# Kernel tuning notes

Hardware: AMD Instinct MI355X
Metric: run time of the kernel (lower is better)

## Reference

```python
import jax, jax.numpy as jnp
import numpy as np

STRIDE = 1
PADDING = 1

def setup_inputs() -> dict:
    key = jax.random.key(0)
    k1, k2, k3 = jax.random.split(key, 3)
    N, C_in, H, W = 32, 128, 56, 56
    C_out, K = 256, 3
    inputs = jax.random.normal(k1, (N, C_in, H, W), dtype=jnp.float32)
    # trunc_normal(std=0.1) approximated by clipped normal
    filters = jnp.clip(jax.random.normal(k2, (C_out, C_in, K, K), dtype=jnp.float32) * 0.1, -0.2, 0.2)
    bias = jnp.clip(jax.random.normal(k3, (C_out,), dtype=jnp.float32) * 0.1, -0.2, 0.2)
    return {"inputs": inputs, "filters": filters, "bias": bias}

def reference(inputs, filters, bias):
    # Equivalent of the quadruple-loop conv: standard cross-correlation,
    # NCHW input, OIHW filters, stride/padding from module config.
    out = jax.lax.conv_general_dilated(
        inputs, filters,
        window_strides=(STRIDE, STRIDE),
        padding=[(PADDING, PADDING), (PADDING, PADDING)],
        dimension_numbers=("NCHW", "OIHW", "NCHW"),
    )
    out = out + bias[None, :, None, None]
    return out
```

## Files before the change

### kernel.cpp

```cpp
#include <hip/hip_runtime.h>

#define CIN    128
#define HH     56
#define WW_    56
#define NBATCH 32
#define COUT   256
#define KTOT   1152
#define PLANE  3136
#define HP     58
#define BM     128
#define BN     128
#define BK     64

#define WB_OFF   0
#define XP_OFF   (1u << 20)

typedef __attribute__((ext_vector_type(8))) short bf16x8;
typedef __attribute__((ext_vector_type(4))) float f32x4;

__device__ __forceinline__ unsigned short f2bf(float f) {
    unsigned int u = __builtin_bit_cast(unsigned int, f);
    u += 0x7fffu + ((u >> 16) & 1u);
    return (unsigned short)(u >> 16);
}

__device__ __forceinline__ void gl_lds16(const void* g, void* l) {
    __builtin_amdgcn_global_load_lds(
        (const __attribute__((address_space(1))) void*)g,
        (__attribute__((address_space(3))) void*)l, 16, 0, 0);
}

__global__ void wprep(const float* __restrict__ w, unsigned short* __restrict__ wb) {
    const int o = blockIdx.x;
    const int t = threadIdx.x;
    const float* src = w + (size_t)o * KTOT;
    unsigned short* dst = wb + (size_t)o * KTOT;
    #pragma unroll
    for (int e = 0; e < 5; ++e) {
        const int idx = t + e * 256;
        if (idx < KTOT) {
            const int ci  = idx / 9;
            const int tap = idx - ci * 9;
            dst[tap * 128 + ci] = f2bf(src[idx]);
        }
    }
}

__global__ __launch_bounds__(256)
void xprep(const float* __restrict__ in, unsigned short* __restrict__ xp) {
    const int b  = blockIdx.x;
    const int n  = b / HP;
    const int ho = b - n * HP;
    const int t  = threadIdx.x;
    uint4* orow = (uint4*)(xp + (((size_t)n * HP + ho) * HP) * CIN);

    if (ho == 0 || ho == HP - 1) {
        #pragma unroll
        for (int e = 0; e < 4; ++e) {
            const int idx = t + e * 256;
            if (idx < 928) orow[idx] = (uint4){0u, 0u, 0u, 0u};
        }
        return;
    }

    __shared__ unsigned short L[CIN * 57];
    const int h  = ho - 1;
    const int w  = t & 63;
    const int cb = t >> 6;
    if (w < WW_) {
        const float* ib = in + ((size_t)n * CIN) * PLANE + (size_t)h * WW_ + w;
        #pragma unroll
        for (int e = 0; e < 32; ++e) {
            const int ci = cb * 32 + e;
            L[ci * 57 + w] = f2bf(ib[(size_t)ci * PLANE]);
        }
    }
    __syncthreads();

    #pragma unroll
    for (int e = 0; e < 4; ++e) {
        const int idx = t + e * 256;
        if (idx < 928) {
            const int wo = idx >> 4;
            const int ch = idx & 15;
            uint4 pk = {0u, 0u, 0u, 0u};
            if (wo >= 1 && wo <= WW_) {
                const int wi = wo - 1;
                unsigned v[8];
                #pragma unroll
                for (int i = 0; i < 8; ++i)
                    v[i] = L[(ch * 8 + i) * 57 + wi];
                pk.x = v[0] | (v[1] << 16);
                pk.y = v[2] | (v[3] << 16);
                pk.z = v[4] | (v[5] << 16);
                pk.w = v[6] | (v[7] << 16);
            }
            orow[idx] = pk;
        }
    }
}

__global__ __launch_bounds__(256, 2)
void conv_mfma(const unsigned short* __restrict__ wb,
               const unsigned short* __restrict__ xp,
               const float* __restrict__ bias,
               float* __restrict__ out)
{
    __shared__ __align__(16) unsigned short Asm_[BM * BK];
    __shared__ __align__(16) unsigned short Bsm_[BN * BK];

    const int t    = threadIdx.x;
    const int pix0 = blockIdx.x * BN;
    const int c0   = blockIdx.y * BM;

    const int slot = t & 7;
    const int r32  = t >> 3;
    const int swiz = (slot ^ (r32 & 7)) * 16;

    const char* aBase = (const char*)wb + (size_t)(c0 + r32) * (KTOT * 2) + swiz;
    const char* bBase[4];
    #pragma unroll
    for (int p = 0; p < 4; ++p) {
        const int pix = pix0 + r32 + p * 32;
        const int n   = pix / PLANE;
        const int rem = pix - n * PLANE;
        const int h   = rem / WW_;
        const int w   = rem - h * WW_;
        bBase[p] = (const char*)xp + ((size_t)(n * HP + h) * HP + w) * (CIN * 2) + swiz;
    }

    const int lane = t & 63;
    const int wave = t >> 6;
    const int wm   = (wave & 1) * 64;
    const int wn   = (wave >> 1) * 64;
    const int lr   = lane & 15;
    const int quad = lane >> 4;
    const int rmod = lr & 7;

    f32x4 acc[4][4];
    #pragma unroll
    for (int i = 0; i < 4; ++i)
        #pragma unroll
        for (int j = 0; j < 4; ++j)
            acc[i][j] = (f32x4){0.f, 0.f, 0.f, 0.f};

    char* const asmb = (char*)Asm_;
    char* const bsmb = (char*)Bsm_;

    for (int tap = 0; tap < 9; ++tap) {
        const int toff = ((tap / 3) * HP + (tap % 3)) * (CIN * 2);
        for (int ci0b = 0; ci0b < 256; ci0b += 128) {
            const int abyte = tap * 256 + ci0b;
            #pragma unroll
            for (int p = 0; p < 4; ++p)
                gl_lds16(aBase + (size_t)p * 32 * (KTOT * 2) + abyte, asmb + p * 4096 + t * 16);
            #pragma unroll
            for (int p = 0; p < 4; ++p)
                gl_lds16(bBase[p] + toff + ci0b, bsmb + p * 4096 + t * 16);
            __syncthreads();

            #pragma unroll
            for (int kk = 0; kk < 2; ++kk) {
                bf16x8 af[4], bfr[4];
                #pragma unroll
                for (int i = 0; i < 4; ++i) {
                    const int r = wm + i * 16 + lr;
                    const int phys = ((kk * 4 + quad) ^ rmod) * 16;
                    af[i] = *(const bf16x8*)(asmb + r * 128 + phys);
                }
                #pragma unroll
                for (int j = 0; j < 4; ++j) {
                    const int r = wn + j * 16 + lr;
                    const int phys = ((kk * 4 + quad) ^ rmod) * 16;
                    bfr[j] = *(const bf16x8*)(bsmb + r * 128 + phys);
                }
                #pragma unroll
                for (int i = 0; i < 4; ++i)
                    #pragma unroll
                    for (int j = 0; j < 4; ++j)
                        acc[i][j] = __builtin_amdgcn_mfma_f32_16x16x32_bf16(af[i], bfr[j], acc[i][j], 0, 0, 0);
            }
            __syncthreads();
        }
    }

    #pragma unroll
    for (int j = 0; j < 4; ++j) {
        const int pg    = pix0 + wn + j * 16 + lr;
        const int ni    = pg / PLANE;
        const int inner = pg - ni * PLANE;
        float* op = out + (size_t)ni * (COUT * PLANE) + inner;
        #pragma unroll
        for (int i = 0; i < 4; ++i) {
            const int crow = c0 + wm + i * 16 + quad * 4;
            #pragma unroll
            for (int r = 0; r < 4; ++r)
                op[(size_t)(crow + r) * PLANE] = acc[i][j][r] + bias[crow + r];
        }
    }
}

extern "C" void kernel_launch(void* const* d_in, const int* in_sizes, int n_in,
                              void* d_out, int out_size, void* d_ws, size_t ws_size,
                              hipStream_t stream) {
    const float* in   = (const float*)d_in[0];
    const float* wt   = (const float*)d_in[1];
    const float* bias = (const float*)d_in[2];
    float* out        = (float*)d_out;

    unsigned short* wb = (unsigned short*)((char*)d_ws + WB_OFF);
    unsigned short* xp = (unsigned short*)((char*)d_ws + XP_OFF);

    wprep<<<COUT, 256, 0, stream>>>(wt, wb);
    xprep<<<NBATCH * HP, 256, 0, stream>>>(in, xp);

    dim3 grid((NBATCH * PLANE) / BN, COUT / BM);
    conv_mfma<<<grid, 256, 0, stream>>>(wb, xp, bias, out);
}
```

Measured before the change: 208.9 us.

## Fuse prep kernels, vectorize input loads, raise occupancy, use nontemporal output stores

Result: slower. 259.4 us (+24.2%).

```diff
diff --git a/kernel.cpp b/kernel.cpp
--- a/kernel.cpp
+++ b/kernel.cpp
@@ -14,6 +14,7 @@
 
 #define WB_OFF   0
 #define XP_OFF   (1u << 20)
+#define LSTR     66
 
 typedef __attribute__((ext_vector_type(8))) short bf16x8;
 typedef __attribute__((ext_vector_type(4))) float f32x4;
@@ -30,28 +31,32 @@
         (__attribute__((address_space(3))) void*)l, 16, 0, 0);
 }
 
-__global__ void wprep(const float* __restrict__ w, unsigned short* __restrict__ wb) {
-    const int o = blockIdx.x;
+__global__ __launch_bounds__(256)
+void prep(const float* __restrict__ in, const float* __restrict__ wt,
+          unsigned short* __restrict__ xp, unsigned short* __restrict__ wb) {
+    const int b = blockIdx.x;
     const int t = threadIdx.x;
-    const float* src = w + (size_t)o * KTOT;
-    unsigned short* dst = wb + (size_t)o * KTOT;
-    #pragma unroll
-    for (int e = 0; e < 5; ++e) {
-        const int idx = t + e * 256;
-        if (idx < KTOT) {
-            const int ci  = idx / 9;
-            const int tap = idx - ci * 9;
-            dst[tap * 128 + ci] = f2bf(src[idx]);
-        }
-    }
-}
-
-__global__ __launch_bounds__(256)
-void xprep(const float* __restrict__ in, unsigned short* __restrict__ xp) {
-    const int b  = blockIdx.x;
+
+    if (b >= NBATCH * HP) {
+        const int o0 = (b - NBATCH * HP) * 8;
+        for (int oo = 0; oo < 8; ++oo) {
+            const float* src = wt + (size_t)(o0 + oo) * KTOT;
+            unsigned short* dst = wb + (size_t)(o0 + oo) * KTOT;
+            #pragma unroll
+            for (int e = 0; e < 5; ++e) {
+                const int idx = t + e * 256;
+                if (idx < KTOT) {
+                    const int ci  = idx / 9;
+                    const int tap = idx - ci * 9;
+                    dst[tap * 128 + ci] = f2bf(src[idx]);
+                }
+            }
+        }
+        return;
+    }
+
     const int n  = b / HP;
     const int ho = b - n * HP;
-    const int t  = threadIdx.x;
     uint4* orow = (uint4*)(xp + (((size_t)n * HP + ho) * HP) * CIN);
 
     if (ho == 0 || ho == HP - 1) {
@@ -63,16 +68,20 @@
         return;
     }
 
-    __shared__ unsigned short L[CIN * 57];
+    __shared__ unsigned short L[CIN * LSTR];
     const int h  = ho - 1;
-    const int w  = t & 63;
-    const int cb = t >> 6;
-    if (w < WW_) {
-        const float* ib = in + ((size_t)n * CIN) * PLANE + (size_t)h * WW_ + w;
-        #pragma unroll
-        for (int e = 0; e < 32; ++e) {
-            const int ci = cb * 32 + e;
-            L[ci * 57 + w] = f2bf(ib[(size_t)ci * PLANE]);
+    const int f4 = t & 15;
+    const int cg = t >> 4;
+    if (f4 < 14) {
+        const float* rowb = in + ((size_t)n * CIN) * PLANE + (size_t)h * WW_;
+        #pragma unroll
+        for (int g = 0; g < 8; ++g) {
+            const int ci = cg + g * 16;
+            const float4 v = *(const float4*)(rowb + (size_t)ci * PLANE + f4 * 4);
+            unsigned lo = (unsigned)f2bf(v.x) | ((unsigned)f2bf(v.y) << 16);
+            unsigned hi = (unsigned)f2bf(v.z) | ((unsigned)f2bf(v.w) << 16);
+            *(unsigned*)&L[ci * LSTR + f4 * 4]     = lo;
+            *(unsigned*)&L[ci * LSTR + f4 * 4 + 2] = hi;
         }
     }
     __syncthreads();
@@ -89,7 +98,7 @@
                 unsigned v[8];
                 #pragma unroll
                 for (int i = 0; i < 8; ++i)
-                    v[i] = L[(ch * 8 + i) * 57 + wi];
+                    v[i] = L[(ch * 8 + i) * LSTR + wi];
                 pk.x = v[0] | (v[1] << 16);
                 pk.y = v[2] | (v[3] << 16);
                 pk.z = v[4] | (v[5] << 16);
@@ -100,7 +109,7 @@
     }
 }
 
-__global__ __launch_bounds__(256, 2)
+__global__ __launch_bounds__(256, 4)
 void conv_mfma(const unsigned short* __restrict__ wb,
                const unsigned short* __restrict__ xp,
                const float* __restrict__ bias,
@@ -195,7 +204,8 @@
             const int crow = c0 + wm + i * 16 + quad * 4;
             #pragma unroll
             for (int r = 0; r < 4; ++r)
-                op[(size_t)(crow + r) * PLANE] = acc[i][j][r] + bias[crow + r];
+                __builtin_nontemporal_store(acc[i][j][r] + bias[crow + r],
+                                            &op[(size_t)(crow + r) * PLANE]);
         }
     }
 }
@@ -211,8 +221,7 @@
     unsigned short* wb = (unsigned short*)((char*)d_ws + WB_OFF);
     unsigned short* xp = (unsigned short*)((char*)d_ws + XP_OFF);
 
-    wprep<<<COUT, 256, 0, stream>>>(wt, wb);
-    xprep<<<NBATCH * HP, 256, 0, stream>>>(in, xp);
+    prep<<<NBATCH * HP + 32, 256, 0, stream>>>(in, wt, xp, wb);
 
     dim3 grid((NBATCH * PLANE) / BN, COUT / BM);
     conv_mfma<<<grid, 256, 0, stream>>>(wb, xp, bias, out);
```
